# Kernel tuning notes

Hardware: AMD Instinct MI355X
Metric: run time of the kernel (lower is better)

The kernel has to match this reference:

```python
import jax, jax.numpy as jnp
import numpy as np


def _rx_gate(weights):
    # Single-qubit Rx gate: cos(w/2) I - i sin(w/2) X  (2x2 complex)
    a = jnp.cos(weights / 2)[0]
    b = jnp.sin(weights / 2)[0]
    eye = jnp.eye(2, dtype=jnp.float32)
    offx = jnp.array([[0.0, 1.0], [1.0, 0.0]], dtype=jnp.float32)
    return (a * eye - 1j * b * offx).astype(jnp.complex64)


def _krons(gate, n_qubits):
    # Recursive Kronecker product of n identical 2x2 gates -> (2^n, 2^n)
    full = gate
    for _ in range(n_qubits - 1):
        full = jnp.kron(full, gate)
    return full


def setup_inputs() -> dict:
    key = jax.random.key(0)
    k1, k2, k3 = jax.random.split(key, 3)
    B, BLK, DC, NQ = 256, 1, 2, 12
    dim = 2 ** NQ  # 4096
    state_re = jax.random.normal(k1, (B, BLK, DC, dim, 1), dtype=jnp.float32)
    state_im = jax.random.normal(k2, (B, BLK, DC, dim, 1), dtype=jnp.float32)
    weights = jax.random.uniform(k3, (1,), dtype=jnp.float32,
                                 minval=-np.pi / 2, maxval=np.pi / 2)
    return {"state_re": state_re, "state_im": state_im,
            "weights": weights, "n_qubits": NQ}


def reference(state_re, state_im, weights, n_qubits):
    gate = _rx_gate(weights)                      # (2, 2) complex64
    full = _krons(gate, n_qubits)                 # (2^n, 2^n) complex64
    state = (state_re + 1j * state_im).astype(jnp.complex64)  # (B,BLK,DC,2^n,1)
    return jnp.matmul(full, state)                # broadcasted dense matmul
```

## Files before the change

### kernel.cpp

```cpp
#include <hip/hip_runtime.h>
#include <hip/hip_bf16.h>


#define DIM 4096
#define NQ 12
#define TPB 256

template <bool INTERLEAVED>
__global__ __launch_bounds__(TPB) void rx_layer_kernel(
    const float* __restrict__ re, const float* __restrict__ im,
    const float* __restrict__ w, float* __restrict__ out)
{
    __shared__ float sre[DIM];
    __shared__ float sim[DIM];

    const int v   = blockIdx.x;
    const int tid = threadIdx.x;

    const float4* re4 = (const float4*)(re + (size_t)v * DIM);
    const float4* im4 = (const float4*)(im + (size_t)v * DIM);
    float4* sre4 = (float4*)sre;
    float4* sim4 = (float4*)sim;
#pragma unroll
    for (int i = tid; i < DIM / 4; i += TPB) {
        sre4[i] = re4[i];
        sim4[i] = im4[i];
    }

    const float half = 0.5f * w[0];
    float ca, sb;
    __sincosf(half, &sb, &ca);
    ca = cosf(half);
    sb = sinf(half);

    __syncthreads();

#pragma unroll
    for (int q = 0; q < NQ; ++q) {
        const int bit  = 1 << q;
        const int mask = bit - 1;
#pragma unroll
        for (int p = tid; p < DIM / 2; p += TPB) {
            const int i0 = ((p & ~mask) << 1) | (p & mask);
            const int i1 = i0 | bit;
            const float r0 = sre[i0], m0 = sim[i0];
            const float r1 = sre[i1], m1 = sim[i1];
            sre[i0] = ca * r0 + sb * m1;
            sim[i0] = ca * m0 - sb * r1;
            sre[i1] = ca * r1 + sb * m0;
            sim[i1] = ca * m1 - sb * r0;
        }
        __syncthreads();
    }

    if (INTERLEAVED) {
        float4* o4 = (float4*)(out + (size_t)v * DIM * 2);
#pragma unroll
        for (int j = tid; j < DIM / 2; j += TPB) {
            const int k = 2 * j;
            o4[j] = make_float4(sre[k], sim[k], sre[k + 1], sim[k + 1]);
        }
    } else {
        float4* o4 = (float4*)(out + (size_t)v * DIM);
#pragma unroll
        for (int i = tid; i < DIM / 4; i += TPB) {
            o4[i] = sre4[i];
        }
    }
}

extern "C" void kernel_launch(void* const* d_in, const int* in_sizes, int n_in,
                              void* d_out, int out_size, void* d_ws, size_t ws_size,
                              hipStream_t stream)
{
    const float* re = (const float*)d_in[0];
    const float* im = (const float*)d_in[1];
    const float* w  = (const float*)d_in[2];
    float* out = (float*)d_out;

    const int nvec = in_sizes[0] / DIM;

    if (out_size == 2 * in_sizes[0]) {
        rx_layer_kernel<true><<<nvec, TPB, 0, stream>>>(re, im, w, out);
    } else {
        rx_layer_kernel<false><<<nvec, TPB, 0, stream>>>(re, im, w, out);
    }
}
```

Measured before the change: 82.01 us.

## Keep state in registers; apply qubit gates via in-register, shuffle, and one LDS exchange

Each thread now keeps 16 complex amplitudes in registers. Four qubits are applied in-thread, six across lanes with xor shuffles, and the two cross-wave qubits through a single shared-memory exchange using a combined 4x4 formula. This replaces twelve shared-memory passes with barriers, cutting LDS traffic and synchronisation. It raises register pressure and relies on a fixed mapping of thread to index bits.

```diff
diff --git a/kernel.cpp b/kernel.cpp
--- a/kernel.cpp
+++ b/kernel.cpp
@@ -3,69 +3,118 @@
 
 
 #define DIM 4096
-#define NQ 12
 #define TPB 256
+
+__device__ __forceinline__ void bf(float ca, float sb,
+                                   float& r0, float& q0, float& r1, float& q1)
+{
+    const float nr0 = ca * r0 + sb * q1;
+    const float nq0 = ca * q0 - sb * r1;
+    const float nr1 = ca * r1 + sb * q0;
+    const float nq1 = ca * q1 - sb * r0;
+    r0 = nr0; q0 = nq0; r1 = nr1; q1 = nq1;
+}
 
 template <bool INTERLEAVED>
 __global__ __launch_bounds__(TPB) void rx_layer_kernel(
     const float* __restrict__ re, const float* __restrict__ im,
     const float* __restrict__ w, float* __restrict__ out)
 {
-    __shared__ float sre[DIM];
-    __shared__ float sim[DIM];
+    __shared__ float lds[32][TPB];
 
-    const int v   = blockIdx.x;
-    const int tid = threadIdx.x;
+    const int v = blockIdx.x;
+    const int t = threadIdx.x;
 
     const float4* re4 = (const float4*)(re + (size_t)v * DIM);
     const float4* im4 = (const float4*)(im + (size_t)v * DIM);
-    float4* sre4 = (float4*)sre;
-    float4* sim4 = (float4*)sim;
+
+    float r[4][4], q[4][4];
 #pragma unroll
-    for (int i = tid; i < DIM / 4; i += TPB) {
-        sre4[i] = re4[i];
-        sim4[i] = im4[i];
+    for (int h = 0; h < 4; ++h) {
+        const float4 a = re4[256 * h + t];
+        const float4 b = im4[256 * h + t];
+        r[h][0] = a.x; r[h][1] = a.y; r[h][2] = a.z; r[h][3] = a.w;
+        q[h][0] = b.x; q[h][1] = b.y; q[h][2] = b.z; q[h][3] = b.w;
     }
 
     const float half = 0.5f * w[0];
-    float ca, sb;
-    __sincosf(half, &sb, &ca);
-    ca = cosf(half);
-    sb = sinf(half);
+    const float ca = cosf(half);
+    const float sb = sinf(half);
 
+#pragma unroll
+    for (int h = 0; h < 4; ++h) {
+        bf(ca, sb, r[h][0], q[h][0], r[h][1], q[h][1]);
+        bf(ca, sb, r[h][2], q[h][2], r[h][3], q[h][3]);
+        bf(ca, sb, r[h][0], q[h][0], r[h][2], q[h][2]);
+        bf(ca, sb, r[h][1], q[h][1], r[h][3], q[h][3]);
+    }
+#pragma unroll
+    for (int c = 0; c < 4; ++c) {
+        bf(ca, sb, r[0][c], q[0][c], r[1][c], q[1][c]);
+        bf(ca, sb, r[2][c], q[2][c], r[3][c], q[3][c]);
+        bf(ca, sb, r[0][c], q[0][c], r[2][c], q[2][c]);
+        bf(ca, sb, r[1][c], q[1][c], r[3][c], q[3][c]);
+    }
+
+#pragma unroll
+    for (int s = 0; s < 6; ++s) {
+        const int m = 1 << s;
+#pragma unroll
+        for (int h = 0; h < 4; ++h)
+#pragma unroll
+            for (int c = 0; c < 4; ++c) {
+                const float rp = __shfl_xor(r[h][c], m, 64);
+                const float qp = __shfl_xor(q[h][c], m, 64);
+                r[h][c] = ca * r[h][c] + sb * qp;
+                q[h][c] = ca * q[h][c] - sb * rp;
+            }
+    }
+
+    const int wv = t >> 6;
+    const int l  = t & 63;
+#pragma unroll
+    for (int h = 0; h < 4; ++h)
+#pragma unroll
+        for (int c = 0; c < 4; ++c) {
+            const int k = (h * 4 + c) * 2;
+            lds[k + 0][t] = r[h][c];
+            lds[k + 1][t] = q[h][c];
+        }
     __syncthreads();
 
+    const float A2 = ca * ca;
+    const float AB = ca * sb;
+    const float B2 = sb * sb;
+    const int p1 = ((wv ^ 1) << 6) | l;
+    const int p2 = ((wv ^ 2) << 6) | l;
+    const int p3 = ((wv ^ 3) << 6) | l;
+
 #pragma unroll
-    for (int q = 0; q < NQ; ++q) {
-        const int bit  = 1 << q;
-        const int mask = bit - 1;
+    for (int h = 0; h < 4; ++h)
 #pragma unroll
-        for (int p = tid; p < DIM / 2; p += TPB) {
-            const int i0 = ((p & ~mask) << 1) | (p & mask);
-            const int i1 = i0 | bit;
-            const float r0 = sre[i0], m0 = sim[i0];
-            const float r1 = sre[i1], m1 = sim[i1];
-            sre[i0] = ca * r0 + sb * m1;
-            sim[i0] = ca * m0 - sb * r1;
-            sre[i1] = ca * r1 + sb * m0;
-            sim[i1] = ca * m1 - sb * r0;
+        for (int c = 0; c < 4; ++c) {
+            const int k = (h * 4 + c) * 2;
+            const float r1 = lds[k][p1],     r2 = lds[k][p2],     r3 = lds[k][p3];
+            const float q1 = lds[k + 1][p1], q2 = lds[k + 1][p2], q3 = lds[k + 1][p3];
+            const float nr = A2 * r[h][c] + AB * (q1 + q2) - B2 * r3;
+            const float nq = A2 * q[h][c] - AB * (r1 + r2) - B2 * q3;
+            r[h][c] = nr;
+            q[h][c] = nq;
         }
-        __syncthreads();
-    }
 
     if (INTERLEAVED) {
-        float4* o4 = (float4*)(out + (size_t)v * DIM * 2);
+        float* o = out + (size_t)v * DIM * 2;
 #pragma unroll
-        for (int j = tid; j < DIM / 2; j += TPB) {
-            const int k = 2 * j;
-            o4[j] = make_float4(sre[k], sim[k], sre[k + 1], sim[k + 1]);
+        for (int h = 0; h < 4; ++h) {
+            float4* o4 = (float4*)(o + 2048 * h + 8 * t);
+            o4[0] = make_float4(r[h][0], q[h][0], r[h][1], q[h][1]);
+            o4[1] = make_float4(r[h][2], q[h][2], r[h][3], q[h][3]);
         }
     } else {
         float4* o4 = (float4*)(out + (size_t)v * DIM);
 #pragma unroll
-        for (int i = tid; i < DIM / 4; i += TPB) {
-            o4[i] = sre4[i];
-        }
+        for (int h = 0; h < 4; ++h)
+            o4[256 * h + t] = make_float4(r[h][0], r[h][1], r[h][2], r[h][3]);
     }
 }
 
```

Measured after the change: 76.20 us. 7.1% less time.
